# Optimization experiments

Hardware: AMD Instinct MI355X
Metric: run time of the kernel (lower is better)

## Reference

```python
import jax, jax.numpy as jnp
import numpy as np

S, B, I, H, L = 512, 64, 512, 512, 2
EPS = 1e-5


def setup_inputs() -> dict:
    key = jax.random.key(0)
    ks = jax.random.split(key, 8)
    gain = float(np.sqrt(1.0 / H))
    u = lambda k, shp: jax.random.uniform(k, shp, jnp.float32, -gain, gain)
    return {
        "inputs": jax.random.normal(ks[0], (S, B, I), jnp.float32),
        "h0": jnp.zeros((L, B, H), jnp.float32),
        "c0": jnp.zeros((L, B, H), jnp.float32),
        "wx0": u(ks[1], (I, 4 * H)),
        "wx1": u(ks[2], (H, 4 * H)),
        "wh0": u(ks[3], (H, 4 * H)),
        "wh1": u(ks[4], (H, 4 * H)),
        "bias": u(ks[5], (L, 4 * H)),
        "ln_gamma": jnp.ones((L, 4, H), jnp.float32),
        "ln_beta": jnp.zeros((L, 4, H), jnp.float32),
    }


def _layer(x, h, c, wx, wh, b, gamma, beta):
    # Precompute the input projection as one big GEMM: [S,B,4H]
    xg = jnp.einsum('sbi,ig->sbg', x, wx) + b

    def cell(carry, xg_t):
        h, c = carry
        gate = xg_t + h @ wh                      # [B, 4H]
        g = gate.reshape(B, 4, H)
        mu = jnp.mean(g, axis=-1, keepdims=True)
        var = jnp.var(g, axis=-1, keepdims=True)
        g = (g - mu) * jax.lax.rsqrt(var + EPS) * gamma + beta
        i, f, o, u = g[:, 0], g[:, 1], g[:, 2], g[:, 3]
        c = jax.nn.sigmoid(f) * c + jax.nn.sigmoid(i) * jnp.tanh(u)
        h = jax.nn.sigmoid(o) * jnp.tanh(c)
        return (h, c), h

    (h, c), ys = jax.lax.scan(cell, (h, c), xg)
    return ys, h, c


def reference(inputs, h0, c0, wx0, wx1, wh0, wh1, bias, ln_gamma, ln_beta):
    x = inputs
    wxs, whs = [wx0, wx1], [wh0, wh1]
    hs, cs = [], []
    for l in range(L):
        x, h, c = _layer(x, h0[l], c0[l], wxs[l], whs[l], bias[l], ln_gamma[l], ln_beta[l])
        hs.append(h)
        cs.append(c)
    return x, jnp.stack(hs, 0), jnp.stack(cs, 0)
```

## Files before the change

### kernel.cpp

```cpp
#include <hip/hip_runtime.h>


#define NTH 256

typedef float f32x4 __attribute__((ext_vector_type(4)));

__device__ __forceinline__ float sigm(float x) { return 1.f / (1.f + __expf(-x)); }
__device__ __forceinline__ float tanh_f(float x) { return 2.f / (1.f + __expf(-2.f * x)) - 1.f; }

__device__ __forceinline__ unsigned long long pack2(float a, float b) {
  union { float f[2]; unsigned long long u; } x; x.f[0] = a; x.f[1] = b; return x.u;
}
__device__ __forceinline__ float lo2(unsigned long long u) {
  union { unsigned long long u; float f[2]; } x; x.u = u; return x.f[0];
}
__device__ __forceinline__ float hi2(unsigned long long u) {
  union { unsigned long long u; float f[2]; } x; x.u = u; return x.f[1];
}

__device__ __forceinline__ void sys_store64(unsigned long long* p, unsigned long long v) {
  __hip_atomic_store(p, v, __ATOMIC_RELAXED, __HIP_MEMORY_SCOPE_SYSTEM);
}
__device__ __forceinline__ unsigned long long sys_load64(const unsigned long long* p) {
  return __hip_atomic_load(p, __ATOMIC_RELAXED, __HIP_MEMORY_SCOPE_SYSTEM);
}

__device__ __forceinline__ void post(unsigned int* flag, unsigned int val) {
  __syncthreads();
  if (threadIdx.x == 0)
    __hip_atomic_store(flag, val, __ATOMIC_RELEASE, __HIP_MEMORY_SCOPE_SYSTEM);
}

__device__ __forceinline__ void waitall(const unsigned int* flags, unsigned int target) {
  long guard = 0;
  for (;;) {
    int ok = 1;
    if (threadIdx.x < 128) {
      unsigned int v = __hip_atomic_load(&flags[threadIdx.x * 32],
                                         __ATOMIC_RELAXED, __HIP_MEMORY_SCOPE_SYSTEM);
      ok = (v >= target);
    }
    if (__syncthreads_and(ok)) break;
    if (++guard > (1L << 22)) break;
  }
  __atomic_signal_fence(__ATOMIC_ACQUIRE);
}

__global__ __launch_bounds__(NTH, 1)
void lstm_pk(const float* __restrict__ inputs, const float* __restrict__ h0,
             const float* __restrict__ c0,
             const float* __restrict__ wx0, const float* __restrict__ wx1,
             const float* __restrict__ wh0, const float* __restrict__ wh1,
             const float* __restrict__ bias, const float* __restrict__ gamma_,
             const float* __restrict__ beta_,
             float* __restrict__ out,
             unsigned int* flags,
             unsigned long long* slots,
             unsigned long long* minv_g,
             float* __restrict__ h_state)
{
  extern __shared__ float lds[];
  float* W_lds = lds;
  float* A_lds = lds + 16384;
  float* part  = lds + 16384 + 17408;
  float* gates = part + 4352;
  float* minv  = gates + 1024;

  const int tid = threadIdx.x;
  const int wg = blockIdx.x;
  const int layer = wg >> 7;
  const int w = wg & 127;
  const int wavet = tid >> 6;
  const int lane = tid & 63;
  const int rq = lane & 15;
  const int gq = lane >> 4;
  const int srow = tid >> 2;
  const int sg = tid & 3;
  const int hc = 4 * w + sg;

  const float* Wx = layer ? wx1 : wx0;
  const float* Wh = layer ? wh1 : wh0;

  for (int i = 0; i < 16; ++i) {
    int e = tid + i * 256;
    int k = e >> 2, g = e & 3;
    const float* src = (k < 512) ? (Wx + (size_t)k * 2048)
                                 : (Wh + (size_t)(k - 512) * 2048);
    f32x4 v = *(const f32x4*)(src + g * 512 + 4 * w);
    *(f32x4*)&W_lds[k * 16 + g * 4] = v;
  }

  f32x4 biasr = *(const f32x4*)(bias + layer * 2048 + sg * 512 + 4 * w);
  float gam[4], bet[4];
#pragma unroll
  for (int g = 0; g < 4; ++g) {
    gam[g] = gamma_[layer * 2048 + g * 512 + hc];
    bet[g] = beta_[layer * 2048 + g * 512 + hc];
  }
  float c_st = c0[layer * 32768 + srow * 512 + hc];

  unsigned long long* slotL = slots + (size_t)layer * 32768;
  unsigned long long* minvL = minv_g + layer * 256;
  float* hstL = h_state + layer * 32768;
  unsigned int* fmyL = flags + layer * 4096;
  unsigned int* myflag = fmyL + w * 32;
  const unsigned int* fL0 = flags;

  const int strow = rq + 16 * wavet;
  const int first = layer ? 4 : 0;

  for (int t = 0; t < 512; ++t) {
    const unsigned int t3 = 3u * (unsigned)t;
    const float* xsrc = (layer ? out : inputs) + (size_t)t * 32768;
    const float* hsrc = (t == 0) ? (h0 + layer * 32768) : hstL;

    if (layer == 1 && t > 0) {
      waitall(fmyL, t3);
      __builtin_amdgcn_fence(__ATOMIC_ACQUIRE, "agent");
    }

    f32x4 acc[4];
#pragma unroll
    for (int r = 0; r < 4; ++r) acc[r] = (f32x4){0.f, 0.f, 0.f, 0.f};

    f32x4 st[8];
    auto LOADC = [&](int c) {
      const float* src = (c >= 4) ? hsrc : xsrc;
      const int koff = (c & 3) * 128;
#pragma unroll
      for (int i = 0; i < 8; ++i) {
        int kq = gq + 4 * i;
        st[i] = *(const f32x4*)(src + strow * 512 + koff + 4 * kq);
      }
    };
    auto WRITEC = [&](int b) {
      float* dst = A_lds + b * 8704;
#pragma unroll
      for (int i = 0; i < 8; ++i) {
        int kq = gq + 4 * i;
#pragma unroll
        for (int j = 0; j < 4; ++j)
          dst[(4 * kq + j) * 68 + strow] = st[i][j];
      }
    };
    auto COMPUTEC = [&](int c, int b) {
      const float* Ab = A_lds + b * 8704;
      const int kg = c * 128 + wavet * 32;
#pragma unroll 8
      for (int kk = 0; kk < 32; ++kk) {
        int k = wavet * 32 + kk;
        f32x4 av = *(const f32x4*)&Ab[k * 68 + 4 * rq];
        f32x4 wv = *(const f32x4*)&W_lds[(kg + kk) * 16 + gq * 4];
        acc[0] += av[0] * wv;
        acc[1] += av[1] * wv;
        acc[2] += av[2] * wv;
        acc[3] += av[3] * wv;
      }
    };

    LOADC(first);
    WRITEC(0);
    __syncthreads();
#pragma unroll 1
    for (int co = 0; co < 8; ++co) {
      int c = (co + first) & 7;
      if (co < 7) {
        if (co == 3) {
          if (layer == 1) {
            waitall(fL0, t3 + 3u);
            __builtin_amdgcn_fence(__ATOMIC_ACQUIRE, "agent");
          } else if (t > 0) {
            waitall(fmyL, t3);
            __builtin_amdgcn_fence(__ATOMIC_ACQUIRE, "agent");
          }
        }
        LOADC((c + 1) & 7);
      }
      COMPUTEC(c, co & 1);
      if (co < 7) WRITEC((co + 1) & 1);
      __syncthreads();
    }

#pragma unroll
    for (int r = 0; r < 4; ++r)
#pragma unroll
      for (int cc = 0; cc < 4; ++cc)
        part[(wavet * 64 + 4 * rq + r) * 17 + gq * 4 + cc] = acc[r][cc];
    __syncthreads();

    {
      f32x4 pre;
#pragma unroll
      for (int cc = 0; cc < 4; ++cc) {
        float v = biasr[cc];
        v += part[(0 * 64 + srow) * 17 + sg * 4 + cc];
        v += part[(1 * 64 + srow) * 17 + sg * 4 + cc];
        v += part[(2 * 64 + srow) * 17 + sg * 4 + cc];
        v += part[(3 * 64 + srow) * 17 + sg * 4 + cc];
        pre[cc] = v;
      }
      *(f32x4*)&gates[srow * 16 + sg * 4] = pre;
      float s = ((pre[0] + pre[1]) + pre[2]) + pre[3];
      float ss = ((pre[0] * pre[0] + pre[1] * pre[1]) + pre[2] * pre[2]) + pre[3] * pre[3];
      sys_store64(&slotL[(size_t)tid * 128 + w], pack2(s, ss));
    }
    post(myflag, t3 + 1u);
    waitall(fmyL, t3 + 1u);

    if (tid < 128) {
      const int pr = 2 * w + (tid >> 6);
      unsigned long long a = sys_load64(&slotL[(size_t)pr * 128 + lane]);
      unsigned long long b = sys_load64(&slotL[(size_t)pr * 128 + lane + 64]);
      float s = lo2(a) + lo2(b);
      float ss = hi2(a) + hi2(b);
#pragma unroll
      for (int k2 = 0; k2 < 6; ++k2) {
        s += __shfl_xor(s, 1 << k2);
        ss += __shfl_xor(ss, 1 << k2);
      }
      if (lane == 0) {
        float mu = s * (1.f / 512.f);
        float var = ss * (1.f / 512.f) - mu * mu;
        float inv = rsqrtf(fmaxf(var, 0.f) + 1e-5f);
        sys_store64(&minvL[pr], pack2(mu, inv));
      }
    }
    post(myflag, t3 + 2u);
    waitall(fmyL, t3 + 2u);

    if (tid < 128) {
#pragma unroll
      for (int j = 0; j < 2; ++j) {
        int pr = tid + 128 * j;
        unsigned long long u = sys_load64(&minvL[pr]);
        minv[pr * 2 + 0] = lo2(u);
        minv[pr * 2 + 1] = hi2(u);
      }
    }
    __syncthreads();

    {
      float gv[4];
#pragma unroll
      for (int g = 0; g < 4; ++g) {
        float pre = gates[srow * 16 + g * 4 + sg];
        gv[g] = (pre - minv[(srow * 4 + g) * 2]) * minv[(srow * 4 + g) * 2 + 1] * gam[g] + bet[g];
      }
      float ig = sigm(gv[0]);
      float fg = sigm(gv[1]);
      float og = sigm(gv[2]);
      float ug = tanh_f(gv[3]);
      c_st = fg * c_st + ig * ug;
      float hv = og * tanh_f(c_st);

      float hv2 = __shfl_down(hv, 1);
      float cv2 = __shfl_down(c_st, 1);
      if ((sg & 1) == 0) {
        unsigned long long hp = pack2(hv, hv2);
        sys_store64((unsigned long long*)&hstL[srow * 512 + hc], hp);
        sys_store64((unsigned long long*)&out[(size_t)t * 32768 + srow * 512 + hc], hp);
        if (t == 511) {
          sys_store64((unsigned long long*)&out[16777216 + layer * 32768 + srow * 512 + hc], hp);
          sys_store64((unsigned long long*)&out[16842752 + layer * 32768 + srow * 512 + hc],
                      pack2(c_st, cv2));
        }
      }
    }
    post(myflag, t3 + 3u);
  }
}

extern "C" void kernel_launch(void* const* d_in, const int* in_sizes, int n_in,
                              void* d_out, int out_size, void* d_ws, size_t ws_size,
                              hipStream_t stream) {
  const float* inputs = (const float*)d_in[0];
  const float* h0 = (const float*)d_in[1];
  const float* c0 = (const float*)d_in[2];
  const float* wx0 = (const float*)d_in[3];
  const float* wx1 = (const float*)d_in[4];
  const float* wh0 = (const float*)d_in[5];
  const float* wh1 = (const float*)d_in[6];
  const float* bias = (const float*)d_in[7];
  const float* gamma_ = (const float*)d_in[8];
  const float* beta_ = (const float*)d_in[9];
  float* out = (float*)d_out;

  char* ws = (char*)d_ws;
  unsigned int* flags = (unsigned int*)ws;
  unsigned long long* slots = (unsigned long long*)(ws + 65536);
  unsigned long long* minv_g = (unsigned long long*)(ws + 65536 + 524288);
  float* h_state = (float*)(ws + 65536 + 524288 + 4096);

  const int smem_bytes = 158720;
  hipFuncSetAttribute((const void*)lstm_pk,
                      hipFuncAttributeMaxDynamicSharedMemorySize, smem_bytes);
  hipMemsetAsync(ws, 0, 65536, stream);

  hipLaunchKernelGGL(lstm_pk, dim3(256), dim3(NTH), smem_bytes, stream,
                     inputs, h0, c0, wx0, wx1, wh0, wh1, bias, gamma_, beta_,
                     out, flags, slots, minv_g, h_state);
}
```

Before: 20.27 ms.

## Replace two-phase LayerNorm stats reduction with redundant per-block reduction, dropping a barrier

Measured after the change: 21.61 ms. +6.6%, slower.

```diff
diff --git a/kernel.cpp b/kernel.cpp
--- a/kernel.cpp
+++ b/kernel.cpp
@@ -17,7 +17,6 @@
 __device__ __forceinline__ float hi2(unsigned long long u) {
   union { unsigned long long u; float f[2]; } x; x.u = u; return x.f[1];
 }
-
 __device__ __forceinline__ void sys_store64(unsigned long long* p, unsigned long long v) {
   __hip_atomic_store(p, v, __ATOMIC_RELAXED, __HIP_MEMORY_SCOPE_SYSTEM);
 }
@@ -56,7 +55,6 @@
              float* __restrict__ out,
              unsigned int* flags,
              unsigned long long* slots,
-             unsigned long long* minv_g,
              float* __restrict__ h_state)
 {
   extern __shared__ float lds[];
@@ -100,7 +98,6 @@
   float c_st = c0[layer * 32768 + srow * 512 + hc];
 
   unsigned long long* slotL = slots + (size_t)layer * 32768;
-  unsigned long long* minvL = minv_g + layer * 256;
   float* hstL = h_state + layer * 32768;
   unsigned int* fmyL = flags + layer * 4096;
   unsigned int* myflag = fmyL + w * 32;
@@ -110,14 +107,11 @@
   const int first = layer ? 4 : 0;
 
   for (int t = 0; t < 512; ++t) {
-    const unsigned int t3 = 3u * (unsigned)t;
+    const unsigned int t2 = 2u * (unsigned)t;
     const float* xsrc = (layer ? out : inputs) + (size_t)t * 32768;
     const float* hsrc = (t == 0) ? (h0 + layer * 32768) : hstL;
 
-    if (layer == 1 && t > 0) {
-      waitall(fmyL, t3);
-      __builtin_amdgcn_fence(__ATOMIC_ACQUIRE, "agent");
-    }
+    if (layer == 1 && t > 0) waitall(fmyL, t2);
 
     f32x4 acc[4];
 #pragma unroll
@@ -125,12 +119,25 @@
 
     f32x4 st[8];
     auto LOADC = [&](int c) {
-      const float* src = (c >= 4) ? hsrc : xsrc;
       const int koff = (c & 3) * 128;
-#pragma unroll
-      for (int i = 0; i < 8; ++i) {
-        int kq = gq + 4 * i;
-        st[i] = *(const f32x4*)(src + strow * 512 + koff + 4 * kq);
+      if (c < 4 && layer == 0) {
+        const float* src = xsrc + strow * 512 + koff;
+#pragma unroll
+        for (int i = 0; i < 8; ++i) {
+          int kq = gq + 4 * i;
+          st[i] = *(const f32x4*)(src + 4 * kq);
+        }
+      } else {
+        const float* src = ((c >= 4) ? hsrc : xsrc) + strow * 512 + koff;
+        const unsigned long long* s64 = (const unsigned long long*)src;
+#pragma unroll
+        for (int i = 0; i < 8; ++i) {
+          int kq = gq + 4 * i;
+          unsigned long long a = sys_load64(&s64[2 * kq]);
+          unsigned long long b = sys_load64(&s64[2 * kq + 1]);
+          st[i][0] = lo2(a); st[i][1] = hi2(a);
+          st[i][2] = lo2(b); st[i][3] = hi2(b);
+        }
       }
     };
     auto WRITEC = [&](int b) {
@@ -166,13 +173,8 @@
       int c = (co + first) & 7;
       if (co < 7) {
         if (co == 3) {
-          if (layer == 1) {
-            waitall(fL0, t3 + 3u);
-            __builtin_amdgcn_fence(__ATOMIC_ACQUIRE, "agent");
-          } else if (t > 0) {
-            waitall(fmyL, t3);
-            __builtin_amdgcn_fence(__ATOMIC_ACQUIRE, "agent");
-          }
+          if (layer == 1) waitall(fL0, t2 + 2u);
+          else if (t > 0) waitall(fmyL, t2);
         }
         LOADC((c + 1) & 7);
       }
@@ -202,40 +204,29 @@
       *(f32x4*)&gates[srow * 16 + sg * 4] = pre;
       float s = ((pre[0] + pre[1]) + pre[2]) + pre[3];
       float ss = ((pre[0] * pre[0] + pre[1] * pre[1]) + pre[2] * pre[2]) + pre[3] * pre[3];
-      sys_store64(&slotL[(size_t)tid * 128 + w], pack2(s, ss));
-    }
-    post(myflag, t3 + 1u);
-    waitall(fmyL, t3 + 1u);
-
-    if (tid < 128) {
-      const int pr = 2 * w + (tid >> 6);
-      unsigned long long a = sys_load64(&slotL[(size_t)pr * 128 + lane]);
-      unsigned long long b = sys_load64(&slotL[(size_t)pr * 128 + lane + 64]);
-      float s = lo2(a) + lo2(b);
-      float ss = hi2(a) + hi2(b);
-#pragma unroll
-      for (int k2 = 0; k2 < 6; ++k2) {
-        s += __shfl_xor(s, 1 << k2);
-        ss += __shfl_xor(ss, 1 << k2);
-      }
-      if (lane == 0) {
-        float mu = s * (1.f / 512.f);
-        float var = ss * (1.f / 512.f) - mu * mu;
-        float inv = rsqrtf(fmaxf(var, 0.f) + 1e-5f);
-        sys_store64(&minvL[pr], pack2(mu, inv));
-      }
-    }
-    post(myflag, t3 + 2u);
-    waitall(fmyL, t3 + 2u);
-
-    if (tid < 128) {
-#pragma unroll
-      for (int j = 0; j < 2; ++j) {
-        int pr = tid + 128 * j;
-        unsigned long long u = sys_load64(&minvL[pr]);
-        minv[pr * 2 + 0] = lo2(u);
-        minv[pr * 2 + 1] = hi2(u);
-      }
+      sys_store64(&slotL[(size_t)w * 256 + tid], pack2(s, ss));
+    }
+    post(myflag, t2 + 1u);
+    waitall(fmyL, t2 + 1u);
+
+    {
+      float Sc[8], SSc[8];
+#pragma unroll
+      for (int j = 0; j < 8; ++j) { Sc[j] = 0.f; SSc[j] = 0.f; }
+#pragma unroll 4
+      for (int q8 = 0; q8 < 16; ++q8) {
+#pragma unroll
+        for (int j = 0; j < 8; ++j) {
+          unsigned long long u = sys_load64(&slotL[(size_t)(q8 * 8 + j) * 256 + tid]);
+          Sc[j] += lo2(u); SSc[j] += hi2(u);
+        }
+      }
+      float S = ((Sc[0] + Sc[1]) + (Sc[2] + Sc[3])) + ((Sc[4] + Sc[5]) + (Sc[6] + Sc[7]));
+      float SS = ((SSc[0] + SSc[1]) + (SSc[2] + SSc[3])) + ((SSc[4] + SSc[5]) + (SSc[6] + SSc[7]));
+      float mu = S * (1.f / 512.f);
+      float var = SS * (1.f / 512.f) - mu * mu;
+      minv[tid * 2 + 0] = mu;
+      minv[tid * 2 + 1] = rsqrtf(fmaxf(var, 0.f) + 1e-5f);
     }
     __syncthreads();
 
@@ -266,7 +257,7 @@
         }
       }
     }
-    post(myflag, t3 + 3u);
+    post(myflag, t2 + 2u);
   }
 }
 
@@ -288,8 +279,7 @@
   char* ws = (char*)d_ws;
   unsigned int* flags = (unsigned int*)ws;
   unsigned long long* slots = (unsigned long long*)(ws + 65536);
-  unsigned long long* minv_g = (unsigned long long*)(ws + 65536 + 524288);
-  float* h_state = (float*)(ws + 65536 + 524288 + 4096);
+  float* h_state = (float*)(ws + 65536 + 524288);
 
   const int smem_bytes = 158720;
   hipFuncSetAttribute((const void*)lstm_pk,
@@ -298,5 +288,5 @@
 
   hipLaunchKernelGGL(lstm_pk, dim3(256), dim3(NTH), smem_bytes, stream,
                      inputs, h0, c0, wx0, wx1, wh0, wh1, bias, gamma_, beta_,
-                     out, flags, slots, minv_g, h_state);
-}
+                     out, flags, slots, h_state);
+}
```
